# Optimization experiments

Hardware: AMD Instinct MI355X
Metric: run time of the kernel (lower is better)

## Reference

```python
import jax, jax.numpy as jnp
import numpy as np

B, S, DIN, DQ, DK = 4, 2048, 1024, 64, 64
NEG_INF = -jnp.inf


def _make_mask(sq, sk):
    # Mirrors createMask: causal mask (-inf where key_idx > query_idx),
    # except 3 randomly chosen (row, col) 'global token' pairs left at 0.
    # torch version uses random.sample; we use a fixed numpy RNG for determinism.
    rng = np.random.default_rng(0)
    g_rows = rng.choice(sk, 3, replace=False)  # sampled from range(lrlen)
    g_cols = rng.choice(sq, 3, replace=False)  # sampled from range(sequence_len)
    row = jnp.arange(sq)[:, None]
    col = jnp.arange(sk)[None, :]
    mask = jnp.where(col > row, NEG_INF, 0.0).astype(jnp.float32)
    mask = mask.at[jnp.asarray(g_rows), jnp.asarray(g_cols)].set(0.0)
    return mask  # [sq, sk]


def setup_inputs() -> dict:
    key = jax.random.key(0)
    ks = jax.random.split(key, 9)
    sc = 1.0 / np.sqrt(DIN)
    return {
        "q": jax.random.normal(ks[0], (B, S, DIN), jnp.float32),
        "k": jax.random.normal(ks[1], (B, S, DIN), jnp.float32),
        "v": jax.random.normal(ks[2], (B, S, DIN), jnp.float32),
        "Wq": jax.random.normal(ks[3], (DIN, DQ), jnp.float32) * sc,
        "bq": jax.random.normal(ks[4], (DQ,), jnp.float32) * sc,
        "Wk": jax.random.normal(ks[5], (DIN, DK), jnp.float32) * sc,
        "bk": jax.random.normal(ks[6], (DK,), jnp.float32) * sc,
        "Wv": jax.random.normal(ks[7], (DIN, DK), jnp.float32) * sc,
        "bv": jax.random.normal(ks[8], (DK,), jnp.float32) * sc,
    }


def reference(q, k, v, Wq, bq, Wk, bk, Wv, bv):
    Q = q @ Wq + bq            # [B,S,DQ]
    K = k @ Wk + bk            # [B,S,DK]
    V = v @ Wv + bv            # [B,S,DK]
    scores = jnp.einsum("bqd,bkd->bqk", Q, K)  # [B,S,S]
    mask = _make_mask(scores.shape[-2], scores.shape[-1])
    denom = jnp.asarray(K.shape[-1], jnp.float32) ** 0.5
    # NOTE: original adds mask BEFORE dividing by sqrt(d_k); -inf survives division.
    attn = jax.nn.softmax((scores + mask) / denom, axis=-1)
    return jnp.einsum("bqk,bkd->bqd", attn, V)  # [B,S,DK]
```

## Files before the change

### kernel.cpp

```cpp
#include <hip/hip_runtime.h>
#include <cstdint>
#include <cstddef>
#include <math.h>

#define SEQ    2048
#define NBATCH 4
#define DIN    1024
#define DH     64

typedef __attribute__((ext_vector_type(8))) short  short8;
typedef __attribute__((ext_vector_type(4))) float  floatx4;
typedef __attribute__((ext_vector_type(4))) unsigned short ushort4v;

#define MFMA16(a, b, c) __builtin_amdgcn_mfma_f32_16x16x32_bf16((a), (b), (c), 0, 0, 0)

__device__ __forceinline__ unsigned short f2bf(float x) {
  unsigned u = __float_as_uint(x);
  return (unsigned short)((u + 0x8000u) >> 16);
}
__device__ __forceinline__ float bf2f(unsigned short h) {
  return __uint_as_float(((unsigned)h) << 16);
}

__device__ __forceinline__ void async_cp4(const void* g, void* l) {
  __builtin_amdgcn_global_load_lds(
      (const __attribute__((address_space(1))) void*)g,
      (__attribute__((address_space(3))) void*)l, 4, 0, 0);
}
__device__ __forceinline__ void async_cp16(const void* g, void* l) {
  __builtin_amdgcn_global_load_lds(
      (const __attribute__((address_space(1))) void*)g,
      (__attribute__((address_space(3))) void*)l, 16, 0, 0);
}

namespace nprng {

struct PCG64 {
  __uint128_t state, inc;
  bool has_uint32;
  uint32_t uinteger;
};

static inline void pcg_step(PCG64 &g) {
  const __uint128_t MULT =
      (((__uint128_t)0x2360ed051fc65da4ULL) << 64) | 0x4385df649fccf645ULL;
  g.state = g.state * MULT + g.inc;
}

static inline uint64_t pcg_output(const PCG64 &g) {
  uint64_t hi = (uint64_t)(g.state >> 64);
  uint64_t lo = (uint64_t)g.state;
  uint64_t x = hi ^ lo;
  unsigned rot = (unsigned)(g.state >> 122) & 63u;
  return (x >> rot) | (x << ((64u - rot) & 63u));
}

static inline uint64_t pcg_next64(PCG64 &g) { pcg_step(g); return pcg_output(g); }

static inline uint32_t pcg_next32(PCG64 &g) {
  if (g.has_uint32) { g.has_uint32 = false; return g.uinteger; }
  uint64_t n = pcg_next64(g);
  g.has_uint32 = true;
  g.uinteger = (uint32_t)(n >> 32);
  return (uint32_t)(n & 0xffffffffu);
}

static inline void pcg_seed_from_seedseq0(PCG64 &g) {
  const uint32_t MULT_A = 0x931e8875u;
  const uint32_t MULT_B = 0x58f38dedu;
  const uint32_t MIX_L  = 0xca01f9ddu;
  const uint32_t MIX_R  = 0x4973f715u;
  uint32_t hc = 0x43b0d7e5u;
  uint32_t pool[4];
  for (int i = 0; i < 4; i++) {
    uint32_t v = 0u;
    v ^= hc; hc *= MULT_A; v *= hc; v ^= v >> 16;
    pool[i] = v;
  }
  for (int is = 0; is < 4; is++) {
    for (int id = 0; id < 4; id++) {
      if (is == id) continue;
      uint32_t h = pool[is];
      h ^= hc; hc *= MULT_A; h *= hc; h ^= h >> 16;
      uint32_t r = (pool[id] * MIX_L) ^ (h * MIX_R);
      r ^= r >> 16;
      pool[id] = r;
    }
  }
  uint32_t hb = 0x8b51f9ddu;
  uint32_t w[8];
  for (int i = 0; i < 8; i++) {
    uint32_t v = pool[i & 3];
    v ^= hb; hb *= MULT_B; v *= hb; v ^= v >> 16;
    w[i] = v;
  }
  uint64_t sv[4];
  for (int k = 0; k < 4; k++)
    sv[k] = (uint64_t)w[2 * k] | ((uint64_t)w[2 * k + 1] << 32);
  __uint128_t initstate = (((__uint128_t)sv[0]) << 64) | sv[1];
  __uint128_t initseq   = (((__uint128_t)sv[2]) << 64) | sv[3];
  g.state = 0; g.inc = (initseq << 1) | 1;
  pcg_step(g);
  g.state += initstate;
  pcg_step(g);
  g.has_uint32 = false; g.uinteger = 0;
}

static inline uint32_t bounded32(PCG64 &g, uint32_t rng ) {
  if (rng == 0) return 0;
  const uint32_t rng_excl = rng + 1u;
  uint64_t m = (uint64_t)pcg_next32(g) * (uint64_t)rng_excl;
  uint32_t leftover = (uint32_t)m;
  if (leftover < rng_excl) {
    const uint32_t threshold = (uint32_t)(0xffffffffu - rng) % rng_excl;
    while (leftover < threshold) {
      m = (uint64_t)pcg_next32(g) * (uint64_t)rng_excl;
      leftover = (uint32_t)m;
    }
  }
  return (uint32_t)(m >> 32);
}

static inline void choice3_2048(PCG64 &g, long long idx[3]) {
  const int pop = 2048, sz = 3;
  uint64_t hs[4] = { (uint64_t)-1, (uint64_t)-1, (uint64_t)-1, (uint64_t)-1 };
  const uint64_t mask = 3;
  for (int j = pop - sz; j < pop; j++) {
    uint64_t val = (uint64_t)bounded32(g, (uint32_t)j);
    uint64_t loc = val & mask;
    while (hs[loc] != (uint64_t)-1 && hs[loc] != val) loc = (loc + 1) & mask;
    if (hs[loc] == (uint64_t)-1) {
      hs[loc] = val;
      idx[j - pop + sz] = (long long)val;
    } else {
      loc = (uint64_t)j & mask;
      while (hs[loc] != (uint64_t)-1) loc = (loc + 1) & mask;
      hs[loc] = (uint64_t)j;
      idx[j - pop + sz] = (long long)j;
    }
  }
  for (int i = 2; i >= 1; i--) {
    uint32_t j = bounded32(g, (uint32_t)i);
    long long t = idx[j]; idx[j] = idx[i]; idx[i] = t;
  }
}

}

__global__ __launch_bounds__(256) void wtrans_kernel(
    const float* __restrict__ Wq, const float* __restrict__ Wk,
    const float* __restrict__ Wv, unsigned short* __restrict__ WTc) {
  int idx = blockIdx.x * 256 + threadIdx.x;
  int p   = idx >> 16;
  int rem = idx & 65535;
  int n   = rem >> 10;
  int k   = rem & 1023;
  const float* W = (p == 0) ? Wq : (p == 1) ? Wk : Wv;
  unsigned short v = f2bf(W[k * 64 + n]);
  int dst = ((p * 8 + (k >> 7)) * 64 + n) * 128 + (k & 127);
  WTc[dst] = v;
}

__global__ __launch_bounds__(256, 2) void proj_kernel(
    const float* __restrict__ xq, const float* __restrict__ xk,
    const float* __restrict__ xv, const unsigned short* __restrict__ WTc,
    const float* __restrict__ bq, const float* __restrict__ bk,
    const float* __restrict__ bv,
    unsigned short* __restrict__ Qf, unsigned short* __restrict__ Kf,
    unsigned short* __restrict__ Vf) {
  const int m0g  = blockIdx.x * 32;
  const int proj = m0g >> 13;
  const int m0   = m0g & 8191;
  const float* X    = (proj == 0) ? xq : (proj == 1) ? xk : xv;
  const float* bias = (proj == 0) ? bq : (proj == 1) ? bk : bv;

  const int tid  = threadIdx.x;
  const int w    = tid >> 6;
  const int l    = tid & 63;
  const int quad = l >> 4;
  const int lx   = l & 15;
  const int mr   = (w & 1) * 16;
  const int nc   = (w >> 1) * 32;

  __shared__ __align__(16) char LDSbuf[2 * 16896 + 2 * 16640];

  const float* Xblk = X + (size_t)m0 * DIN;
  const unsigned short* Wpj = WTc + (size_t)proj * 8 * 8192;

  floatx4 acc0 = {0.f, 0.f, 0.f, 0.f}, acc1 = acc0;

  auto stage = [&](int kc, int buf) {
    float* Xs = (float*)(LDSbuf + buf * 16896);
    unsigned short* Ws = (unsigned short*)(LDSbuf + 2 * 16896 + buf * 16640);
#pragma unroll
    for (int i = 0; i < 8; i++) {
      const int r = 8 * w + i;
      const float* g = Xblk + (size_t)r * DIN + kc * 128;
      async_cp4(g + l,      &Xs[r * 132]);
      async_cp4(g + 64 + l, &Xs[r * 132 + 64]);
    }
#pragma unroll
    for (int i = 0; i < 4; i++) {
      const int g4 = 4 * w + i;
      const unsigned short* gsrc = Wpj + (size_t)kc * 8192 + g4 * 512;
      async_cp16((const char*)gsrc + l * 16, &Ws[g4 * 520]);
    }
  };

  stage(0, 0);
  for (int kc = 0; kc < 8; kc++) {
    __syncthreads();
    if (kc < 7) stage(kc + 1, (kc + 1) & 1);
    const float* Xs = (const float*)(LDSbuf + (kc & 1) * 16896);
    const unsigned short* Ws =
        (const unsigned short*)(LDSbuf + 2 * 16896 + (kc & 1) * 16640);
#pragma unroll
    for (int ks = 0; ks < 4; ks++) {
      const float* ap = &Xs[(mr + lx) * 132 + ks * 32 + quad * 8];
      const float4 f0 = *(const float4*)ap;
      const float4 f1 = *(const float4*)(ap + 4);
      short8 a;
      a[0] = f2bf(f0.x); a[1] = f2bf(f0.y); a[2] = f2bf(f0.z); a[3] = f2bf(f0.w);
      a[4] = f2bf(f1.x); a[5] = f2bf(f1.y); a[6] = f2bf(f1.z); a[7] = f2bf(f1.w);
      const int c0 = nc + lx, c1 = nc + 16 + lx;
      const short8 b0 = *(const short8*)&Ws[(c0 >> 2) * 520 + (c0 & 3) * 128 + ks * 32 + quad * 8];
      const short8 b1 = *(const short8*)&Ws[(c1 >> 2) * 520 + (c1 & 3) * 128 + ks * 32 + quad * 8];
      acc0 = MFMA16(a, b0, acc0);
      acc1 = MFMA16(a, b1, acc1);
    }
  }
  __syncthreads();

  float (*Cs)[68] = (float(*)[68])LDSbuf;
  const float bb0 = bias[nc + lx], bb1 = bias[nc + 16 + lx];
#pragma unroll
  for (int i = 0; i < 4; i++) {
    Cs[mr + quad * 4 + i][nc + lx]      = acc0[i] + bb0;
    Cs[mr + quad * 4 + i][nc + 16 + lx] = acc1[i] + bb1;
  }
  __syncthreads();

  const int bq_ = m0 >> 11;
  const int s0  = m0 & 2047;
  if (proj == 0) {
    const int ti = tid >> 7, s = (tid >> 6) & 1, ll = tid & 63;
    const int lxx = ll & 15, qq = ll >> 4;
    short8 v;
#pragma unroll
    for (int j = 0; j < 8; j++) v[j] = (short)f2bf(Cs[ti * 16 + lxx][s * 32 + qq * 8 + j]);
    char* dst = (char*)Qf + ((size_t)(bq_ * 128 + (s0 >> 4) + ti)) * 2048 + s * 1024 + ll * 16;
    *(short8*)dst = v;
  } else if (proj == 1) {
    const int ci = tid >> 7, s = (tid >> 6) & 1, ll = tid & 63;
    const int lxx = ll & 15, qq = ll >> 4;
    const int c = ((s0 >> 4) & 3) + ci;
    short8 v;
#pragma unroll
    for (int j = 0; j < 8; j++) v[j] = (short)f2bf(Cs[ci * 16 + lxx][s * 32 + qq * 8 + j]);
    char* dst = (char*)Kf + ((size_t)(bq_ * 32 + (s0 >> 6))) * 8192 + (c * 2 + s) * 1024 + ll * 16;
    *(short8*)dst = v;
  } else {
    const int c = tid >> 6, ll = tid & 63;
    const int lxx = ll & 15, qq = ll >> 4;
    const int sh = (s0 >> 5) & 1;
    short8 v;
#pragma unroll
    for (int j = 0; j < 8; j++) v[j] = (short)f2bf(Cs[qq * 8 + j][c * 16 + lxx]);
    char* dst = (char*)Vf + ((size_t)(bq_ * 32 + (s0 >> 6))) * 8192 + (sh * 4 + c) * 1024 + ll * 16;
    *(short8*)dst = v;
  }
}

__global__ __launch_bounds__(256, 2) void attn_kernel(
    const unsigned short* __restrict__ Qf, const unsigned short* __restrict__ Kf,
    const unsigned short* __restrict__ Vf, float* __restrict__ out,
    int R0, int C0, int R1, int C1, int R2, int C2) {
  const int b    = blockIdx.y;
  const int bx   = blockIdx.x;
  const int qi   = (bx & 1) ? (127 - (bx >> 1)) : (bx >> 1);
  const int q0   = qi * 16;
  const int tid  = threadIdx.x;
  const int w    = tid >> 6;
  const int l    = tid & 63;
  const int quad = l >> 4;
  const int lx   = l & 15;

  __shared__ unsigned short Ps[4][16][72];
  __shared__ float Os[4][16][64];
  __shared__ float mS[4][16], lS[4][16];
  __shared__ float lgS[3];
  __shared__ int   lgF[3];

  const char* Qc = (const char*)Qf + ((size_t)(b * 128 + qi)) * 2048 + l * 16;
  const short8 aq0 = *(const short8*)Qc;
  const short8 aq1 = *(const short8*)(Qc + 1024);

  floatx4 O[4];
  float m_i[4], l_i[4];
#pragma unroll
  for (int c = 0; c < 4; c++) O[c] = (floatx4){0.f, 0.f, 0.f, 0.f};
#pragma unroll
  for (int i = 0; i < 4; i++) { m_i[i] = -INFINITY; l_i[i] = 0.f; }

  const int T = (q0 + 79) >> 6;

  for (int t = w; t < T; t += 4) {
    const int k0 = t << 6;
    const bool mT = (t == T - 1);

    const char* Kc = (const char*)Kf + ((size_t)(b * 32 + t)) * 8192 + l * 16;
    const char* Vc = (const char*)Vf + ((size_t)(b * 32 + t)) * 8192 + l * 16;
    short8 kf[8], vf[8];
#pragma unroll
    for (int f = 0; f < 8; f++) {
      kf[f] = *(const short8*)(Kc + f * 1024);
      vf[f] = *(const short8*)(Vc + f * 1024);
    }

    floatx4 sc[4];
#pragma unroll
    for (int c = 0; c < 4; c++) {
      sc[c] = (floatx4){0.f, 0.f, 0.f, 0.f};
      sc[c] = MFMA16(aq0, kf[2 * c], sc[c]);
      sc[c] = MFMA16(aq1, kf[2 * c + 1], sc[c]);
    }

    float mt[4], al[4];
#pragma unroll
    for (int i = 0; i < 4; i++) {
      const int rowg = q0 + quad * 4 + i;
      float vmax = -INFINITY;
#pragma unroll
      for (int c = 0; c < 4; c++) {
        float v = sc[c][i] * 0.125f;
        if (mT && (k0 + 16 * c + lx) > rowg) v = -INFINITY;
        sc[c][i] = v;
        vmax = fmaxf(vmax, v);
      }
      mt[i] = vmax;
    }
#pragma unroll
    for (int i = 0; i < 4; i++) {
#pragma unroll
      for (int off = 8; off >= 1; off >>= 1)
        mt[i] = fmaxf(mt[i], __shfl_xor(mt[i], off));
      const float mn = fmaxf(m_i[i], mt[i]);
      al[i] = __expf(m_i[i] - mn);
      m_i[i] = mn;
      float s = 0.f;
#pragma unroll
      for (int c = 0; c < 4; c++) {
        float p = __expf(sc[c][i] - mn);
        Ps[w][quad * 4 + i][16 * c + lx] = f2bf(p);
        s += p;
      }
#pragma unroll
      for (int off = 8; off >= 1; off >>= 1) s += __shfl_xor(s, off);
      l_i[i] = l_i[i] * al[i] + s;
    }
#pragma unroll
    for (int c = 0; c < 4; c++)
#pragma unroll
      for (int i = 0; i < 4; i++) O[c][i] *= al[i];
    asm volatile("" ::: "memory");
    const short8 pf0 = *(const short8*)&Ps[w][lx][quad * 8];
    const short8 pf1 = *(const short8*)&Ps[w][lx][32 + quad * 8];
#pragma unroll
    for (int c = 0; c < 4; c++) {
      O[c] = MFMA16(pf0, vf[c],     O[c]);
      O[c] = MFMA16(pf1, vf[4 + c], O[c]);
    }
  }

  if (lx == 0) {
#pragma unroll
    for (int i = 0; i < 4; i++) {
      mS[w][quad * 4 + i] = m_i[i];
      lS[w][quad * 4 + i] = l_i[i];
    }
  }
#pragma unroll
  for (int c = 0; c < 4; c++)
#pragma unroll
    for (int i = 0; i < 4; i++) Os[w][quad * 4 + i][16 * c + lx] = O[c][i];

  if (w == 0) {
#pragma unroll
    for (int p = 0; p < 3; p++) {
      const int R = (p == 0) ? R0 : (p == 1) ? R1 : R2;
      const int C = (p == 0) ? C0 : (p == 1) ? C1 : C2;
      const int act = (R >= q0 && R < q0 + 16 && C > R);
      float d = 0.f;
      if (act) {
        const int dd = l;
        const char* qa = (const char*)Qf + ((size_t)(b * 128 + (R >> 4))) * 2048 +
                         (dd >> 5) * 1024 + ((R & 15) + ((dd >> 3) & 3) * 16) * 16 + (dd & 7) * 2;
        const char* ka = (const char*)Kf + ((size_t)(b * 32 + (C >> 6))) * 8192 +
                         (((C >> 4) & 3) * 2 + (dd >> 5)) * 1024 +
                         ((C & 15) + ((dd >> 3) & 3) * 16) * 16 + (dd & 7) * 2;
        d = bf2f(*(const unsigned short*)qa) * bf2f(*(const unsigned short*)ka);
#pragma unroll
        for (int off = 32; off >= 1; off >>= 1) d += __shfl_xor(d, off);
        d *= 0.125f;
      }
      if (l == 0) { lgF[p] = act; lgS[p] = d; }
    }
  }
  __syncthreads();

  {
    const int row = tid >> 4;
    const int d0  = (tid & 15) * 4;
    const int Rs[3] = {R0, R1, R2};
    const int Cs3[3] = {C0, C1, C2};

    float mf = -INFINITY;
#pragma unroll
    for (int w4 = 0; w4 < 4; w4++) mf = fmaxf(mf, mS[w4][row]);
#pragma unroll
    for (int p = 0; p < 3; p++)
      if (lgF[p] && (Rs[p] - q0) == row) mf = fmaxf(mf, lgS[p]);

    float lf = 0.f;
    float o0 = 0.f, o1 = 0.f, o2 = 0.f, o3 = 0.f;
#pragma unroll
    for (int w4 = 0; w4 < 4; w4++) {
      const float a = __expf(mS[w4][row] - mf);
      lf += a * lS[w4][row];
      const float* op = &Os[w4][row][d0];
      o0 += a * op[0]; o1 += a * op[1]; o2 += a * op[2]; o3 += a * op[3];
    }
#pragma unroll
    for (int p = 0; p < 3; p++) {
      if (lgF[p] && (Rs[p] - q0) == row) {
        const float pe = __expf(lgS[p] - mf);
        lf += pe;
        const int C = Cs3[p];
        float vv[4];
#pragma unroll
        for (int j = 0; j < 4; j++) {
          const int dim = d0 + j;
          const char* va = (const char*)Vf + ((size_t)(b * 32 + (C >> 6))) * 8192 +
                           (((C >> 5) & 1) * 4 + (dim >> 4)) * 1024 +
                           ((dim & 15) + ((C >> 3) & 3) * 16) * 16 + (C & 7) * 2;
          vv[j] = bf2f(*(const unsigned short*)va);
        }
        o0 += pe * vv[0]; o1 += pe * vv[1]; o2 += pe * vv[2]; o3 += pe * vv[3];
      }
    }
    const float inv = 1.0f / lf;
    float4 r;
    r.x = o0 * inv; r.y = o1 * inv; r.z = o2 * inv; r.w = o3 * inv;
    *(float4*)(out + ((size_t)b * SEQ + q0 + row) * 64 + d0) = r;
  }
}

extern "C" void kernel_launch(void* const* d_in, const int* in_sizes, int n_in,
                              void* d_out, int out_size, void* d_ws,
                              size_t ws_size, hipStream_t stream) {
  const float* xq = (const float*)d_in[0];
  const float* xk = (const float*)d_in[1];
  const float* xv = (const float*)d_in[2];
  const float* Wq = (const float*)d_in[3];
  const float* bq = (const float*)d_in[4];
  const float* Wk = (const float*)d_in[5];
  const float* bk = (const float*)d_in[6];
  const float* Wv = (const float*)d_in[7];
  const float* bv = (const float*)d_in[8];
  float* out = (float*)d_out;

  unsigned short* Qf  = (unsigned short*)d_ws;
  unsigned short* Kf  = Qf + (size_t)NBATCH * SEQ * 64;
  unsigned short* Vf  = Kf + (size_t)NBATCH * SEQ * 64;
  unsigned short* WTc = Vf + (size_t)NBATCH * SEQ * 64;

  nprng::PCG64 g;
  nprng::pcg_seed_from_seedseq0(g);
  long long rows[3], cols[3];
  nprng::choice3_2048(g, rows);
  nprng::choice3_2048(g, cols);

  wtrans_kernel<<<768, 256, 0, stream>>>(Wq, Wk, Wv, WTc);

  proj_kernel<<<768, 256, 0, stream>>>(xq, xk, xv, WTc, bq, bk, bv, Qf, Kf, Vf);

  dim3 agrid(SEQ / 16, NBATCH);
  attn_kernel<<<agrid, 256, 0, stream>>>(
      Qf, Kf, Vf, out, (int)rows[0], (int)cols[0], (int)rows[1], (int)cols[1],
      (int)rows[2], (int)cols[2]);
}
```

Before: 161.0 us.

## Load projection operands straight to registers with pre-fragmented weights, drop LDS staging

```diff
diff --git a/kernel.cpp b/kernel.cpp
--- a/kernel.cpp
+++ b/kernel.cpp
@@ -10,7 +10,6 @@
 
 typedef __attribute__((ext_vector_type(8))) short  short8;
 typedef __attribute__((ext_vector_type(4))) float  floatx4;
-typedef __attribute__((ext_vector_type(4))) unsigned short ushort4v;
 
 #define MFMA16(a, b, c) __builtin_amdgcn_mfma_f32_16x16x32_bf16((a), (b), (c), 0, 0, 0)
 
@@ -20,17 +19,6 @@
 }
 __device__ __forceinline__ float bf2f(unsigned short h) {
   return __uint_as_float(((unsigned)h) << 16);
-}
-
-__device__ __forceinline__ void async_cp4(const void* g, void* l) {
-  __builtin_amdgcn_global_load_lds(
-      (const __attribute__((address_space(1))) void*)g,
-      (__attribute__((address_space(3))) void*)l, 4, 0, 0);
-}
-__device__ __forceinline__ void async_cp16(const void* g, void* l) {
-  __builtin_amdgcn_global_load_lds(
-      (const __attribute__((address_space(1))) void*)g,
-      (__attribute__((address_space(3))) void*)l, 16, 0, 0);
 }
 
 namespace nprng {
@@ -150,27 +138,33 @@
 __global__ __launch_bounds__(256) void wtrans_kernel(
     const float* __restrict__ Wq, const float* __restrict__ Wk,
     const float* __restrict__ Wv, unsigned short* __restrict__ WTc) {
-  int idx = blockIdx.x * 256 + threadIdx.x;
-  int p   = idx >> 16;
-  int rem = idx & 65535;
-  int n   = rem >> 10;
-  int k   = rem & 1023;
+  const int u = blockIdx.x * 256 + threadIdx.x;
+  const int l   = u & 63;
+  const int fi  = (u >> 6) & 7;
+  const int nch = (u >> 9) & 1;
+  const int kc  = (u >> 10) & 7;
+  const int p   = u >> 13;
+  const int f   = fi & 1;
+  const int ks  = fi >> 1;
   const float* W = (p == 0) ? Wq : (p == 1) ? Wk : Wv;
-  unsigned short v = f2bf(W[k * 64 + n]);
-  int dst = ((p * 8 + (k >> 7)) * 64 + n) * 128 + (k & 127);
-  WTc[dst] = v;
-}
-
-__global__ __launch_bounds__(256, 2) void proj_kernel(
+  const int n  = nch * 32 + f * 16 + (l & 15);
+  const int k0 = kc * 128 + ks * 32 + ((l >> 4) * 8);
+  short8 v;
+#pragma unroll
+  for (int j = 0; j < 8; j++) v[j] = (short)f2bf(W[(size_t)(k0 + j) * 64 + n]);
+  *((short8*)WTc + u) = v;
+}
+
+__global__ __launch_bounds__(128, 3) void proj_kernel(
     const float* __restrict__ xq, const float* __restrict__ xk,
     const float* __restrict__ xv, const unsigned short* __restrict__ WTc,
     const float* __restrict__ bq, const float* __restrict__ bk,
     const float* __restrict__ bv,
     unsigned short* __restrict__ Qf, unsigned short* __restrict__ Kf,
     unsigned short* __restrict__ Vf) {
-  const int m0g  = blockIdx.x * 32;
-  const int proj = m0g >> 13;
-  const int m0   = m0g & 8191;
+  const int bid  = blockIdx.x;
+  const int proj = bid >> 9;
+  const int m0   = (bid & 511) << 4;
   const float* X    = (proj == 0) ? xq : (proj == 1) ? xk : xv;
   const float* bias = (proj == 0) ? bq : (proj == 1) ? bk : bv;
 
@@ -179,94 +173,85 @@
   const int l    = tid & 63;
   const int quad = l >> 4;
   const int lx   = l & 15;
-  const int mr   = (w & 1) * 16;
-  const int nc   = (w >> 1) * 32;
-
-  __shared__ __align__(16) char LDSbuf[2 * 16896 + 2 * 16640];
-
-  const float* Xblk = X + (size_t)m0 * DIN;
-  const unsigned short* Wpj = WTc + (size_t)proj * 8 * 8192;
+
+  const float* Xr = X + (size_t)(m0 + lx) * DIN + quad * 8;
+  const short8* W8 = (const short8*)WTc;
 
   floatx4 acc0 = {0.f, 0.f, 0.f, 0.f}, acc1 = acc0;
-
-  auto stage = [&](int kc, int buf) {
-    float* Xs = (float*)(LDSbuf + buf * 16896);
-    unsigned short* Ws = (unsigned short*)(LDSbuf + 2 * 16896 + buf * 16640);
-#pragma unroll
-    for (int i = 0; i < 8; i++) {
-      const int r = 8 * w + i;
-      const float* g = Xblk + (size_t)r * DIN + kc * 128;
-      async_cp4(g + l,      &Xs[r * 132]);
-      async_cp4(g + 64 + l, &Xs[r * 132 + 64]);
-    }
-#pragma unroll
-    for (int i = 0; i < 4; i++) {
-      const int g4 = 4 * w + i;
-      const unsigned short* gsrc = Wpj + (size_t)kc * 8192 + g4 * 512;
-      async_cp16((const char*)gsrc + l * 16, &Ws[g4 * 520]);
+  float4 xa[8], xb[8];
+
+  auto LDX = [&](int kc, float4* xr) {
+#pragma unroll
+    for (int ks = 0; ks < 4; ks++) {
+      const float* p = Xr + kc * 128 + ks * 32;
+      xr[2 * ks]     = *(const float4*)(p);
+      xr[2 * ks + 1] = *(const float4*)(p + 4);
     }
   };
-
-  stage(0, 0);
-  for (int kc = 0; kc < 8; kc++) {
-    __syncthreads();
-    if (kc < 7) stage(kc + 1, (kc + 1) & 1);
-    const float* Xs = (const float*)(LDSbuf + (kc & 1) * 16896);
-    const unsigned short* Ws =
-        (const unsigned short*)(LDSbuf + 2 * 16896 + (kc & 1) * 16640);
+  auto CHUNK = [&](int kc, const float4* xr) {
+    const short8* Wk8 = W8 + ((((size_t)proj * 8 + kc) * 2 + w) * 8) * 64 + l;
+    short8 wf[8];
+#pragma unroll
+    for (int i = 0; i < 8; i++) wf[i] = Wk8[i * 64];
 #pragma unroll
     for (int ks = 0; ks < 4; ks++) {
-      const float* ap = &Xs[(mr + lx) * 132 + ks * 32 + quad * 8];
-      const float4 f0 = *(const float4*)ap;
-      const float4 f1 = *(const float4*)(ap + 4);
+      const float4 f0 = xr[2 * ks], f1 = xr[2 * ks + 1];
       short8 a;
       a[0] = f2bf(f0.x); a[1] = f2bf(f0.y); a[2] = f2bf(f0.z); a[3] = f2bf(f0.w);
       a[4] = f2bf(f1.x); a[5] = f2bf(f1.y); a[6] = f2bf(f1.z); a[7] = f2bf(f1.w);
-      const int c0 = nc + lx, c1 = nc + 16 + lx;
-      const short8 b0 = *(const short8*)&Ws[(c0 >> 2) * 520 + (c0 & 3) * 128 + ks * 32 + quad * 8];
-      const short8 b1 = *(const short8*)&Ws[(c1 >> 2) * 520 + (c1 & 3) * 128 + ks * 32 + quad * 8];
-      acc0 = MFMA16(a, b0, acc0);
-      acc1 = MFMA16(a, b1, acc1);
-    }
+      acc0 = MFMA16(a, wf[ks * 2],     acc0);
+      acc1 = MFMA16(a, wf[ks * 2 + 1], acc1);
+    }
+  };
+
+  LDX(0, xa);
+#pragma unroll
+  for (int kk = 0; kk < 4; kk++) {
+    LDX(2 * kk + 1, xb);
+    CHUNK(2 * kk, xa);
+    if (kk < 3) LDX(2 * kk + 2, xa);
+    CHUNK(2 * kk + 1, xb);
+  }
+
+  __shared__ float Cs[16][68];
+  const float bb0 = bias[w * 32 + lx], bb1 = bias[w * 32 + 16 + lx];
+#pragma unroll
+  for (int i = 0; i < 4; i++) {
+    Cs[quad * 4 + i][w * 32 + lx]      = acc0[i] + bb0;
+    Cs[quad * 4 + i][w * 32 + 16 + lx] = acc1[i] + bb1;
   }
   __syncthreads();
 
-  float (*Cs)[68] = (float(*)[68])LDSbuf;
-  const float bb0 = bias[nc + lx], bb1 = bias[nc + 16 + lx];
-#pragma unroll
-  for (int i = 0; i < 4; i++) {
-    Cs[mr + quad * 4 + i][nc + lx]      = acc0[i] + bb0;
-    Cs[mr + quad * 4 + i][nc + 16 + lx] = acc1[i] + bb1;
-  }
-  __syncthreads();
-
-  const int bq_ = m0 >> 11;
+  const int b_  = m0 >> 11;
   const int s0  = m0 & 2047;
+  const int ll  = tid & 63, lxx = ll & 15, qq = ll >> 4;
+
   if (proj == 0) {
-    const int ti = tid >> 7, s = (tid >> 6) & 1, ll = tid & 63;
-    const int lxx = ll & 15, qq = ll >> 4;
+    const int s = tid >> 6;
     short8 v;
 #pragma unroll
-    for (int j = 0; j < 8; j++) v[j] = (short)f2bf(Cs[ti * 16 + lxx][s * 32 + qq * 8 + j]);
-    char* dst = (char*)Qf + ((size_t)(bq_ * 128 + (s0 >> 4) + ti)) * 2048 + s * 1024 + ll * 16;
+    for (int j = 0; j < 8; j++) v[j] = (short)f2bf(Cs[lxx][s * 32 + qq * 8 + j]);
+    char* dst = (char*)Qf + ((size_t)(b_ * 128 + (s0 >> 4))) * 2048 + s * 1024 + ll * 16;
     *(short8*)dst = v;
   } else if (proj == 1) {
-    const int ci = tid >> 7, s = (tid >> 6) & 1, ll = tid & 63;
-    const int lxx = ll & 15, qq = ll >> 4;
-    const int c = ((s0 >> 4) & 3) + ci;
+    const int s = tid >> 6;
+    const int c = (s0 >> 4) & 3;
     short8 v;
 #pragma unroll
-    for (int j = 0; j < 8; j++) v[j] = (short)f2bf(Cs[ci * 16 + lxx][s * 32 + qq * 8 + j]);
-    char* dst = (char*)Kf + ((size_t)(bq_ * 32 + (s0 >> 6))) * 8192 + (c * 2 + s) * 1024 + ll * 16;
+    for (int j = 0; j < 8; j++) v[j] = (short)f2bf(Cs[lxx][s * 32 + qq * 8 + j]);
+    char* dst = (char*)Kf + ((size_t)(b_ * 32 + (s0 >> 6))) * 8192 + (c * 2 + s) * 1024 + ll * 16;
     *(short8*)dst = v;
   } else {
-    const int c = tid >> 6, ll = tid & 63;
-    const int lxx = ll & 15, qq = ll >> 4;
-    const int sh = (s0 >> 5) & 1;
+    const int h  = (s0 >> 4) & 1;
+    const int sf = (s0 >> 5) & 1;
+    const int c  = tid >> 5;
+    const int lv = h * 32 + (tid & 31);
+    const int q2 = (lv >> 4) & 1;
+    const int lxv = lv & 15;
     short8 v;
 #pragma unroll
-    for (int j = 0; j < 8; j++) v[j] = (short)f2bf(Cs[qq * 8 + j][c * 16 + lxx]);
-    char* dst = (char*)Vf + ((size_t)(bq_ * 32 + (s0 >> 6))) * 8192 + (sh * 4 + c) * 1024 + ll * 16;
+    for (int j = 0; j < 8; j++) v[j] = (short)f2bf(Cs[q2 * 8 + j][c * 16 + lxv]);
+    char* dst = (char*)Vf + ((size_t)(b_ * 32 + (s0 >> 6))) * 8192 + (sf * 4 + c) * 1024 + lv * 16;
     *(short8*)dst = v;
   }
 }
@@ -318,12 +303,14 @@
     }
 
     floatx4 sc[4];
+    __builtin_amdgcn_s_setprio(1);
 #pragma unroll
     for (int c = 0; c < 4; c++) {
       sc[c] = (floatx4){0.f, 0.f, 0.f, 0.f};
       sc[c] = MFMA16(aq0, kf[2 * c], sc[c]);
       sc[c] = MFMA16(aq1, kf[2 * c + 1], sc[c]);
     }
+    __builtin_amdgcn_s_setprio(0);
 
     float mt[4], al[4];
 #pragma unroll
@@ -365,11 +352,13 @@
     asm volatile("" ::: "memory");
     const short8 pf0 = *(const short8*)&Ps[w][lx][quad * 8];
     const short8 pf1 = *(const short8*)&Ps[w][lx][32 + quad * 8];
+    __builtin_amdgcn_s_setprio(1);
 #pragma unroll
     for (int c = 0; c < 4; c++) {
       O[c] = MFMA16(pf0, vf[c],     O[c]);
       O[c] = MFMA16(pf1, vf[4 + c], O[c]);
     }
+    __builtin_amdgcn_s_setprio(0);
   }
 
   if (lx == 0) {
@@ -480,9 +469,9 @@
   nprng::choice3_2048(g, rows);
   nprng::choice3_2048(g, cols);
 
-  wtrans_kernel<<<768, 256, 0, stream>>>(Wq, Wk, Wv, WTc);
-
-  proj_kernel<<<768, 256, 0, stream>>>(xq, xk, xv, WTc, bq, bk, bv, Qf, Kf, Vf);
+  wtrans_kernel<<<96, 256, 0, stream>>>(Wq, Wk, Wv, WTc);
+
+  proj_kernel<<<1536, 128, 0, stream>>>(xq, xk, xv, WTc, bq, bk, bv, Qf, Kf, Vf);
 
   dim3 agrid(SEQ / 16, NBATCH);
   attn_kernel<<<agrid, 256, 0, stream>>>(
```

New measurement: 168.2 us. +4.5%, slower.

## Load projection weights straight to registers in MFMA fragment layout, drop LDS staging

Applied to the files above, without the earlier changes.

```diff
diff --git a/kernel.cpp b/kernel.cpp
--- a/kernel.cpp
+++ b/kernel.cpp
@@ -10,7 +10,6 @@
 
 typedef __attribute__((ext_vector_type(8))) short  short8;
 typedef __attribute__((ext_vector_type(4))) float  floatx4;
-typedef __attribute__((ext_vector_type(4))) unsigned short ushort4v;
 
 #define MFMA16(a, b, c) __builtin_amdgcn_mfma_f32_16x16x32_bf16((a), (b), (c), 0, 0, 0)
 
@@ -27,11 +26,15 @@
       (const __attribute__((address_space(1))) void*)g,
       (__attribute__((address_space(3))) void*)l, 4, 0, 0);
 }
-__device__ __forceinline__ void async_cp16(const void* g, void* l) {
-  __builtin_amdgcn_global_load_lds(
-      (const __attribute__((address_space(1))) void*)g,
-      (__attribute__((address_space(3))) void*)l, 16, 0, 0);
-}
+
+template <int OFF>
+__device__ __forceinline__ void gldw(short8 &d, unsigned long long a) {
+  asm volatile("global_load_dwordx4 %0, %1, off offset:%2"
+               : "=v"(d) : "v"(a), "n"(OFF));
+}
+#define WAITV(N) asm volatile("s_waitcnt vmcnt(" #N ")" ::: "memory")
+#define SB()     __builtin_amdgcn_sched_barrier(0)
+#define BAR()    __builtin_amdgcn_s_barrier()
 
 namespace nprng {
 
@@ -150,18 +153,24 @@
 __global__ __launch_bounds__(256) void wtrans_kernel(
     const float* __restrict__ Wq, const float* __restrict__ Wk,
     const float* __restrict__ Wv, unsigned short* __restrict__ WTc) {
-  int idx = blockIdx.x * 256 + threadIdx.x;
-  int p   = idx >> 16;
-  int rem = idx & 65535;
-  int n   = rem >> 10;
-  int k   = rem & 1023;
+  const int u = blockIdx.x * 256 + threadIdx.x;
+  const int l   = u & 63;
+  const int fi  = (u >> 6) & 7;
+  const int nch = (u >> 9) & 1;
+  const int kc  = (u >> 10) & 7;
+  const int p   = u >> 13;
+  const int f   = fi & 1;
+  const int ks  = fi >> 1;
   const float* W = (p == 0) ? Wq : (p == 1) ? Wk : Wv;
-  unsigned short v = f2bf(W[k * 64 + n]);
-  int dst = ((p * 8 + (k >> 7)) * 64 + n) * 128 + (k & 127);
-  WTc[dst] = v;
-}
-
-__global__ __launch_bounds__(256, 2) void proj_kernel(
+  const int n  = nch * 32 + f * 16 + (l & 15);
+  const int k0 = kc * 128 + ks * 32 + ((l >> 4) * 8);
+  short8 v;
+#pragma unroll
+  for (int j = 0; j < 8; j++) v[j] = (short)f2bf(W[(size_t)(k0 + j) * 64 + n]);
+  *((short8*)WTc + u) = v;
+}
+
+__global__ __launch_bounds__(256, 3) void proj_kernel(
     const float* __restrict__ xq, const float* __restrict__ xk,
     const float* __restrict__ xv, const unsigned short* __restrict__ WTc,
     const float* __restrict__ bq, const float* __restrict__ bk,
@@ -182,54 +191,69 @@
   const int mr   = (w & 1) * 16;
   const int nc   = (w >> 1) * 32;
 
-  __shared__ __align__(16) char LDSbuf[2 * 16896 + 2 * 16640];
+  __shared__ __align__(16) char LDSbuf[2 * 16896];
 
   const float* Xblk = X + (size_t)m0 * DIN;
-  const unsigned short* Wpj = WTc + (size_t)proj * 8 * 8192;
+  const unsigned long long wab =
+      (unsigned long long)(const void*)((const short8*)WTc +
+                                        ((size_t)(proj * 16 + (w >> 1))) * 512 + l);
 
   floatx4 acc0 = {0.f, 0.f, 0.f, 0.f}, acc1 = acc0;
-
-  auto stage = [&](int kc, int buf) {
-    float* Xs = (float*)(LDSbuf + buf * 16896);
-    unsigned short* Ws = (unsigned short*)(LDSbuf + 2 * 16896 + buf * 16640);
-#pragma unroll
-    for (int i = 0; i < 8; i++) {
-      const int r = 8 * w + i;
-      const float* g = Xblk + (size_t)r * DIN + kc * 128;
-      async_cp4(g + l,      &Xs[r * 132]);
-      async_cp4(g + 64 + l, &Xs[r * 132 + 64]);
-    }
-#pragma unroll
-    for (int i = 0; i < 4; i++) {
-      const int g4 = 4 * w + i;
-      const unsigned short* gsrc = Wpj + (size_t)kc * 8192 + g4 * 512;
-      async_cp16((const char*)gsrc + l * 16, &Ws[g4 * 520]);
-    }
-  };
-
-  stage(0, 0);
-  for (int kc = 0; kc < 8; kc++) {
-    __syncthreads();
-    if (kc < 7) stage(kc + 1, (kc + 1) & 1);
-    const float* Xs = (const float*)(LDSbuf + (kc & 1) * 16896);
-    const unsigned short* Ws =
-        (const unsigned short*)(LDSbuf + 2 * 16896 + (kc & 1) * 16640);
-#pragma unroll
-    for (int ks = 0; ks < 4; ks++) {
-      const float* ap = &Xs[(mr + lx) * 132 + ks * 32 + quad * 8];
-      const float4 f0 = *(const float4*)ap;
-      const float4 f1 = *(const float4*)(ap + 4);
-      short8 a;
-      a[0] = f2bf(f0.x); a[1] = f2bf(f0.y); a[2] = f2bf(f0.z); a[3] = f2bf(f0.w);
-      a[4] = f2bf(f1.x); a[5] = f2bf(f1.y); a[6] = f2bf(f1.z); a[7] = f2bf(f1.w);
-      const int c0 = nc + lx, c1 = nc + 16 + lx;
-      const short8 b0 = *(const short8*)&Ws[(c0 >> 2) * 520 + (c0 & 3) * 128 + ks * 32 + quad * 8];
-      const short8 b1 = *(const short8*)&Ws[(c1 >> 2) * 520 + (c1 & 3) * 128 + ks * 32 + quad * 8];
-      acc0 = MFMA16(a, b0, acc0);
-      acc1 = MFMA16(a, b1, acc1);
-    }
-  }
-  __syncthreads();
+  short8  wa[8], wb[8];
+
+#define STAGE(KC, XBUF, WBUF)                                                  \
+  {                                                                            \
+    float* Xs = (float*)(LDSbuf + (XBUF) * 16896);                             \
+    _Pragma("unroll")                                                          \
+    for (int i = 0; i < 8; i++) {                                              \
+      const int r = 8 * w + i;                                                 \
+      const float* g = Xblk + (size_t)r * DIN + (KC) * 128;                    \
+      async_cp4(g + l,      &Xs[r * 132]);                                     \
+      async_cp4(g + 64 + l, &Xs[r * 132 + 64]);                                \
+    }                                                                          \
+    const unsigned long long p0 = wab + (KC) * 16384ull;                       \
+    const unsigned long long p1 = p0 + 4096ull;                                \
+    gldw<   0>(WBUF[0], p0); gldw<1024>(WBUF[1], p0);                          \
+    gldw<2048>(WBUF[2], p0); gldw<3072>(WBUF[3], p0);                          \
+    gldw<   0>(WBUF[4], p1); gldw<1024>(WBUF[5], p1);                          \
+    gldw<2048>(WBUF[6], p1); gldw<3072>(WBUF[7], p1);                          \
+  }
+
+#define CONSUME(XBUF, WBUF)                                                    \
+  {                                                                            \
+    const float* Xs = (const float*)(LDSbuf + (XBUF) * 16896);                 \
+    _Pragma("unroll")                                                          \
+    for (int ks = 0; ks < 4; ks++) {                                           \
+      const float* ap = &Xs[(mr + lx) * 132 + ks * 32 + quad * 8];             \
+      const float4 f0 = *(const float4*)ap;                                    \
+      const float4 f1 = *(const float4*)(ap + 4);                              \
+      short8 a;                                                                \
+      a[0] = f2bf(f0.x); a[1] = f2bf(f0.y); a[2] = f2bf(f0.z); a[3] = f2bf(f0.w); \
+      a[4] = f2bf(f1.x); a[5] = f2bf(f1.y); a[6] = f2bf(f1.z); a[7] = f2bf(f1.w); \
+      acc0 = MFMA16(a, WBUF[2 * ks],     acc0);                                \
+      acc1 = MFMA16(a, WBUF[2 * ks + 1], acc1);                                \
+    }                                                                          \
+  }
+
+  STAGE(0, 0, wa);
+  STAGE(1, 1, wb);
+  WAITV(24); SB(); BAR(); CONSUME(0, wa); BAR();
+  STAGE(2, 0, wa);
+  WAITV(24); SB(); BAR(); CONSUME(1, wb); BAR();
+  STAGE(3, 1, wb);
+  WAITV(24); SB(); BAR(); CONSUME(0, wa); BAR();
+  STAGE(4, 0, wa);
+  WAITV(24); SB(); BAR(); CONSUME(1, wb); BAR();
+  STAGE(5, 1, wb);
+  WAITV(24); SB(); BAR(); CONSUME(0, wa); BAR();
+  STAGE(6, 0, wa);
+  WAITV(24); SB(); BAR(); CONSUME(1, wb); BAR();
+  STAGE(7, 1, wb);
+  WAITV(24); SB(); BAR(); CONSUME(0, wa); BAR();
+  WAITV(0);  SB(); BAR(); CONSUME(1, wb);
+
+#undef STAGE
+#undef CONSUME
 
   float (*Cs)[68] = (float(*)[68])LDSbuf;
   const float bb0 = bias[nc + lx], bb1 = bias[nc + 16 + lx];
@@ -318,12 +342,14 @@
     }
 
     floatx4 sc[4];
+    __builtin_amdgcn_s_setprio(1);
 #pragma unroll
     for (int c = 0; c < 4; c++) {
       sc[c] = (floatx4){0.f, 0.f, 0.f, 0.f};
       sc[c] = MFMA16(aq0, kf[2 * c], sc[c]);
       sc[c] = MFMA16(aq1, kf[2 * c + 1], sc[c]);
     }
+    __builtin_amdgcn_s_setprio(0);
 
     float mt[4], al[4];
 #pragma unroll
@@ -365,11 +391,13 @@
     asm volatile("" ::: "memory");
     const short8 pf0 = *(const short8*)&Ps[w][lx][quad * 8];
     const short8 pf1 = *(const short8*)&Ps[w][lx][32 + quad * 8];
+    __builtin_amdgcn_s_setprio(1);
 #pragma unroll
     for (int c = 0; c < 4; c++) {
       O[c] = MFMA16(pf0, vf[c],     O[c]);
       O[c] = MFMA16(pf1, vf[4 + c], O[c]);
     }
+    __builtin_amdgcn_s_setprio(0);
   }
 
   if (lx == 0) {
@@ -480,7 +508,7 @@
   nprng::choice3_2048(g, rows);
   nprng::choice3_2048(g, cols);
 
-  wtrans_kernel<<<768, 256, 0, stream>>>(Wq, Wk, Wv, WTc);
+  wtrans_kernel<<<96, 256, 0, stream>>>(Wq, Wk, Wv, WTc);
 
   proj_kernel<<<768, 256, 0, stream>>>(xq, xk, xv, WTc, bq, bk, bv, Qf, Kf, Vf);
 
```

Result: faster. 155.0 us (-3.7%).
